# Optimization experiments

Hardware: AMD Instinct MI355X
Metric: run time of the kernel (lower is better)

The kernel has to match this reference:

```python
import jax, jax.numpy as jnp
import numpy as np

NEG_INF = -10000.0
START_TAG = -2  # index into tag axis
END_TAG = -1


def setup_inputs() -> dict:
    B, T, N = 512, 1024, 64
    key = jax.random.key(0)
    k_h, k_tr, k_len = jax.random.split(key, 3)
    h = jax.random.normal(k_h, (B, T, N), dtype=jnp.float32)
    trans = jax.random.normal(k_tr, (N, N), dtype=jnp.float32)
    lengths = jax.random.randint(k_len, (B,), 1, T + 1)
    lengths = lengths.at[0].set(T)  # ensure max(lengths) == T, as the torch loop assumes
    return {"h": h, "trans": trans, "lengths": lengths}


def reference(h, trans, lengths):
    # h: [B, T, N] emissions; trans: [N, N], trans[i, j] = score(j -> i); lengths: [B]
    B, T, N = h.shape
    mask = jnp.arange(T)[None, :] < lengths[:, None]  # [B, T]

    init = jnp.full((B, N), NEG_INF, dtype=h.dtype).at[:, START_TAG].set(0.0)

    def step(score, xs):
        emit_t, m_t = xs  # emit_t: [B, N], m_t: [B]
        # score_t[b, i] = logsumexp_j( score[b, j] + emit_t[b, i] + trans[i, j] )
        s = score[:, None, :] + emit_t[:, :, None] + trans[None, :, :]  # [B, N, N]
        s = jax.nn.logsumexp(s, axis=2)  # [B, N]
        score = jnp.where(m_t[:, None], s, score)
        return score, None

    score, _ = jax.lax.scan(step, init, (jnp.swapaxes(h, 0, 1), mask.T))
    # terminal transition to END tag, then log-partition
    return jax.nn.logsumexp(score + trans[END_TAG], axis=-1)  # [B]
```

## Files before the change

### kernel.cpp

```cpp
#include <hip/hip_runtime.h>

#define LOG2E 1.4426950408889634f
#define LN2   0.6931471805599453f

typedef float f32x2 __attribute__((ext_vector_type(2)));

template <bool FWD>
__device__ __forceinline__ void run_chain(
    const float* __restrict__ hb, const float* __restrict__ trans,
    float* __restrict__ pbuf, int lane, int len, int nsteps, int& b2Out) {
  constexpr int N = 64;

  f32x2 Mp[N / 2];
  if (FWD) {
    const float4* trow = (const float4*)(trans + lane * N);
#pragma unroll
    for (int q = 0; q < 16; ++q) {
      float4 tq = trow[q];
      Mp[2 * q + 0] = {__builtin_amdgcn_exp2f(tq.x * LOG2E),
                       __builtin_amdgcn_exp2f(tq.y * LOG2E)};
      Mp[2 * q + 1] = {__builtin_amdgcn_exp2f(tq.z * LOG2E),
                       __builtin_amdgcn_exp2f(tq.w * LOG2E)};
    }
  } else {
#pragma unroll
    for (int q = 0; q < 32; ++q) {
      Mp[q] = {__builtin_amdgcn_exp2f(trans[(2 * q + 0) * N + lane] * LOG2E),
               __builtin_amdgcn_exp2f(trans[(2 * q + 1) * N + lane] * LOG2E)};
    }
  }
#pragma unroll
  for (int q = 0; q < 8; ++q) {
    asm volatile("" : "+v"(Mp[4 * q + 0]), "+v"(Mp[4 * q + 1]),
                      "+v"(Mp[4 * q + 2]), "+v"(Mp[4 * q + 3]));
  }

  {
    float v;
    if (FWD) {
      v = __builtin_amdgcn_exp2f((hb[lane] + trans[lane * N + (N - 2)]) * LOG2E);
    } else {
      v = __builtin_amdgcn_exp2f(trans[(N - 1) * N + lane] * LOG2E);
      if (nsteps >= 1)
        v *= __builtin_amdgcn_exp2f(hb[(size_t)(len - 1) * N + lane] * LOG2E);
    }
    pbuf[lane] = v;
  }
  int base2 = 0;

  const int ns = FWD ? nsteps : nsteps - 1;

  auto step = [&](float D, bool resc) {
    const float4* pb4 = (const float4*)pbuf;
    f32x2 a0 = {0.f, 0.f}, a1 = {0.f, 0.f}, a2 = {0.f, 0.f}, a3 = {0.f, 0.f};
    float p0ref = 0.f;
#pragma unroll
    for (int g = 0; g < 16; ++g) {
      float4 q = pb4[g];
      if (g == 0) p0ref = q.x;
      f32x2 qlo = {q.x, q.y}, qhi = {q.z, q.w};
      if ((g & 1) == 0) {
        a0 = __builtin_elementwise_fma(Mp[2 * g + 0], qlo, a0);
        a1 = __builtin_elementwise_fma(Mp[2 * g + 1], qhi, a1);
      } else {
        a2 = __builtin_elementwise_fma(Mp[2 * g + 0], qlo, a2);
        a3 = __builtin_elementwise_fma(Mp[2 * g + 1], qhi, a3);
      }
    }
    float mult = D;
    if (resc) {
      unsigned bits = __float_as_uint(p0ref);
      int e = (int)((bits >> 23) & 0xffu);
      base2 += e - 127;
      mult *= __uint_as_float((unsigned)(254 - e) << 23);
    }
    f32x2 s01 = a0 + a1, s23 = a2 + a3;
    f32x2 s2 = s01 + s23;
    pbuf[lane] = (s2.x + s2.y) * mult;
  };

  auto emit_of = [&](int s_) -> float {
    int smax = ns < 1 ? 1 : ns;
    int sc = s_ < smax ? s_ : smax;
    if (sc < 1) sc = 1;
    int t = FWD ? sc : (len - 1 - sc);
    if (t < 0) t = 0;
    return __builtin_amdgcn_exp2f(hb[(size_t)t * N + lane] * LOG2E);
  };

  float eb[8];
#pragma unroll
  for (int u = 0; u < 8; ++u) eb[u] = emit_of(1 + u);

  int s = 1;
  for (; s + 8 <= ns + 1; s += 8) {
#pragma unroll
    for (int u = 0; u < 8; ++u) {
      step(eb[u], (u & 1) == 1);
      eb[u] = emit_of(s + u + 8);
    }
  }
  for (; s <= ns; ++s) {
    step(eb[(s - 1) & 7], true);
  }
  if (!FWD && nsteps >= 1) step(1.0f, true);

  b2Out = base2;
}

__global__ __launch_bounds__(128)
__attribute__((amdgpu_waves_per_eu(1, 1)))
void crf_fwd_33852932227637(
    const float* __restrict__ h,
    const float* __restrict__ trans,
    const int* __restrict__ lengths,
    float* __restrict__ out,
    int T) {
  constexpr int N = 64;
  const int b = blockIdx.x;
  const int lane = threadIdx.x & 63;
  const int wv = threadIdx.x >> 6;

  const float* hb = h + (size_t)b * T * N;
  const int len = lengths[b];
  const int m = (len - 1) >> 1;

  __shared__ __align__(16) float pbuf[2][N];
  __shared__ int xb2[2];

  int b2;
  if (wv == 0)
    run_chain<true>(hb, trans, pbuf[0], lane, len, m, b2);
  else
    run_chain<false>(hb, trans, pbuf[1], lane, len, len - 1 - m, b2);
  if (lane == 0) xb2[wv] = b2;
  __syncthreads();

  if (wv == 0) {
    float z = pbuf[0][lane] * pbuf[1][lane];
#pragma unroll
    for (int off = 32; off >= 1; off >>= 1)
      z += __shfl_xor(z, off, 64);
    if (lane == 0)
      out[b] = LN2 * ((float)(xb2[0] + xb2[1]) + __builtin_amdgcn_logf(z));
  }
}

extern "C" void kernel_launch(void* const* d_in, const int* in_sizes, int n_in,
                              void* d_out, int out_size, void* d_ws, size_t ws_size,
                              hipStream_t stream) {
  const float* h = (const float*)d_in[0];
  const float* trans = (const float*)d_in[1];
  const int* lengths = (const int*)d_in[2];
  float* out = (float*)d_out;
  const int B = in_sizes[2];
  const int N = 64;
  const int T = in_sizes[0] / (B * N);
  crf_fwd_33852932227637<<<B, N * 2, 0, stream>>>(h, trans, lengths, out, T);
}
```

Measured before the change: 240.5 us.

## Split each state's reduction across lane pairs with DPP xor-1 combine

Each lane now computes partial dot products for two output states (k and k+32) over half of the previous-state vector, and a DPP quad-permute adds the two halves from neighbouring lanes. The aim is to halve the LDS reads per lane per step (8 float4 instead of 16) and shorten the serial FMA chain on the latency-bound recurrence. In exchange each step adds a DPP exchange, two LDS stores per lane, and a separate anchor read for rescaling. The emission prefetch depth also drops from 8 to 4 steps, with two emissions loaded per step.

Measured after the change: 248.5 us. 1.03x slower.

```diff
diff --git a/kernel.cpp b/kernel.cpp
--- a/kernel.cpp
+++ b/kernel.cpp
@@ -5,34 +5,52 @@
 
 typedef float f32x2 __attribute__((ext_vector_type(2)));
 
+__device__ __forceinline__ float dpp_xor1(float v) {
+  return __int_as_float(
+      __builtin_amdgcn_mov_dpp(__float_as_int(v), 0xB1, 0xf, 0xf, true));
+}
+
 template <bool FWD>
 __device__ __forceinline__ void run_chain(
     const float* __restrict__ hb, const float* __restrict__ trans,
     float* __restrict__ pbuf, int lane, int len, int nsteps, int& b2Out) {
   constexpr int N = 64;
+  const int k = lane >> 1;
+  const int jh = lane & 1;
 
-  f32x2 Mp[N / 2];
+  f32x2 MpA[16], MpB[16];
   if (FWD) {
-    const float4* trow = (const float4*)(trans + lane * N);
+    const float4* trA = (const float4*)(trans + k * N + 32 * jh);
+    const float4* trB = (const float4*)(trans + (k + 32) * N + 32 * jh);
 #pragma unroll
-    for (int q = 0; q < 16; ++q) {
-      float4 tq = trow[q];
-      Mp[2 * q + 0] = {__builtin_amdgcn_exp2f(tq.x * LOG2E),
-                       __builtin_amdgcn_exp2f(tq.y * LOG2E)};
-      Mp[2 * q + 1] = {__builtin_amdgcn_exp2f(tq.z * LOG2E),
-                       __builtin_amdgcn_exp2f(tq.w * LOG2E)};
+    for (int q = 0; q < 8; ++q) {
+      float4 ta = trA[q];
+      MpA[2 * q + 0] = {__builtin_amdgcn_exp2f(ta.x * LOG2E),
+                        __builtin_amdgcn_exp2f(ta.y * LOG2E)};
+      MpA[2 * q + 1] = {__builtin_amdgcn_exp2f(ta.z * LOG2E),
+                        __builtin_amdgcn_exp2f(ta.w * LOG2E)};
+      float4 tb = trB[q];
+      MpB[2 * q + 0] = {__builtin_amdgcn_exp2f(tb.x * LOG2E),
+                        __builtin_amdgcn_exp2f(tb.y * LOG2E)};
+      MpB[2 * q + 1] = {__builtin_amdgcn_exp2f(tb.z * LOG2E),
+                        __builtin_amdgcn_exp2f(tb.w * LOG2E)};
     }
   } else {
 #pragma unroll
-    for (int q = 0; q < 32; ++q) {
-      Mp[q] = {__builtin_amdgcn_exp2f(trans[(2 * q + 0) * N + lane] * LOG2E),
-               __builtin_amdgcn_exp2f(trans[(2 * q + 1) * N + lane] * LOG2E)};
+    for (int q = 0; q < 16; ++q) {
+      int j0 = 32 * jh + 2 * q, j1 = j0 + 1;
+      MpA[q] = {__builtin_amdgcn_exp2f(trans[j0 * N + k] * LOG2E),
+                __builtin_amdgcn_exp2f(trans[j1 * N + k] * LOG2E)};
+      MpB[q] = {__builtin_amdgcn_exp2f(trans[j0 * N + (k + 32)] * LOG2E),
+                __builtin_amdgcn_exp2f(trans[j1 * N + (k + 32)] * LOG2E)};
     }
   }
 #pragma unroll
-  for (int q = 0; q < 8; ++q) {
-    asm volatile("" : "+v"(Mp[4 * q + 0]), "+v"(Mp[4 * q + 1]),
-                      "+v"(Mp[4 * q + 2]), "+v"(Mp[4 * q + 3]));
+  for (int q = 0; q < 4; ++q) {
+    asm volatile("" : "+v"(MpA[4 * q + 0]), "+v"(MpA[4 * q + 1]),
+                      "+v"(MpA[4 * q + 2]), "+v"(MpA[4 * q + 3]));
+    asm volatile("" : "+v"(MpB[4 * q + 0]), "+v"(MpB[4 * q + 1]),
+                      "+v"(MpB[4 * q + 2]), "+v"(MpB[4 * q + 3]));
   }
 
   {
@@ -50,60 +68,66 @@
 
   const int ns = FWD ? nsteps : nsteps - 1;
 
-  auto step = [&](float D, bool resc) {
-    const float4* pb4 = (const float4*)pbuf;
-    f32x2 a0 = {0.f, 0.f}, a1 = {0.f, 0.f}, a2 = {0.f, 0.f}, a3 = {0.f, 0.f};
-    float p0ref = 0.f;
-#pragma unroll
-    for (int g = 0; g < 16; ++g) {
-      float4 q = pb4[g];
-      if (g == 0) p0ref = q.x;
-      f32x2 qlo = {q.x, q.y}, qhi = {q.z, q.w};
-      if ((g & 1) == 0) {
-        a0 = __builtin_elementwise_fma(Mp[2 * g + 0], qlo, a0);
-        a1 = __builtin_elementwise_fma(Mp[2 * g + 1], qhi, a1);
-      } else {
-        a2 = __builtin_elementwise_fma(Mp[2 * g + 0], qlo, a2);
-        a3 = __builtin_elementwise_fma(Mp[2 * g + 1], qhi, a3);
-      }
-    }
-    float mult = D;
+  const float4* pb4 = (const float4*)pbuf + 8 * jh;
+
+  auto step = [&](float DA, float DB, bool resc) {
+    float mult = 1.0f;
     if (resc) {
-      unsigned bits = __float_as_uint(p0ref);
+      float anch = pbuf[0];
+      unsigned bits = __float_as_uint(anch);
       int e = (int)((bits >> 23) & 0xffu);
       base2 += e - 127;
-      mult *= __uint_as_float((unsigned)(254 - e) << 23);
+      mult = __uint_as_float((unsigned)(254 - e) << 23);
     }
-    f32x2 s01 = a0 + a1, s23 = a2 + a3;
-    f32x2 s2 = s01 + s23;
-    pbuf[lane] = (s2.x + s2.y) * mult;
+    f32x2 a0 = {0.f, 0.f}, a1 = {0.f, 0.f};
+    f32x2 b0 = {0.f, 0.f}, b1 = {0.f, 0.f};
+#pragma unroll
+    for (int g = 0; g < 8; ++g) {
+      float4 q = pb4[g];
+      f32x2 qlo = {q.x, q.y}, qhi = {q.z, q.w};
+      a0 = __builtin_elementwise_fma(MpA[2 * g + 0], qlo, a0);
+      a1 = __builtin_elementwise_fma(MpA[2 * g + 1], qhi, a1);
+      b0 = __builtin_elementwise_fma(MpB[2 * g + 0], qlo, b0);
+      b1 = __builtin_elementwise_fma(MpB[2 * g + 1], qhi, b1);
+    }
+    f32x2 sa = a0 + a1;
+    float pa = sa.x + sa.y;
+    float sumA = pa + dpp_xor1(pa);
+    f32x2 sb = b0 + b1;
+    float pb = sb.x + sb.y;
+    float sumB = pb + dpp_xor1(pb);
+    pbuf[k]      = sumA * (DA * mult);
+    pbuf[k + 32] = sumB * (DB * mult);
   };
 
-  auto emit_of = [&](int s_) -> float {
+  auto emit_of = [&](int s_, int state) -> float {
     int smax = ns < 1 ? 1 : ns;
     int sc = s_ < smax ? s_ : smax;
     if (sc < 1) sc = 1;
     int t = FWD ? sc : (len - 1 - sc);
     if (t < 0) t = 0;
-    return __builtin_amdgcn_exp2f(hb[(size_t)t * N + lane] * LOG2E);
+    return __builtin_amdgcn_exp2f(hb[(size_t)t * N + state] * LOG2E);
   };
 
-  float eb[8];
+  float ebA[4], ebB[4];
 #pragma unroll
-  for (int u = 0; u < 8; ++u) eb[u] = emit_of(1 + u);
+  for (int u = 0; u < 4; ++u) {
+    ebA[u] = emit_of(1 + u, k);
+    ebB[u] = emit_of(1 + u, k + 32);
+  }
 
   int s = 1;
-  for (; s + 8 <= ns + 1; s += 8) {
+  for (; s + 4 <= ns + 1; s += 4) {
 #pragma unroll
-    for (int u = 0; u < 8; ++u) {
-      step(eb[u], (u & 1) == 1);
-      eb[u] = emit_of(s + u + 8);
+    for (int u = 0; u < 4; ++u) {
+      step(ebA[u], ebB[u], (u & 1) == 1);
+      ebA[u] = emit_of(s + u + 4, k);
+      ebB[u] = emit_of(s + u + 4, k + 32);
     }
   }
-  for (; s <= ns; ++s) {
-    step(eb[(s - 1) & 7], true);
-  }
-  if (!FWD && nsteps >= 1) step(1.0f, true);
+  for (; s <= ns; ++s)
+    step(ebA[(s - 1) & 3], ebB[(s - 1) & 3], true);
+  if (!FWD && nsteps >= 1) step(1.0f, 1.0f, true);
 
   b2Out = base2;
 }
```
